# Kernel optimization log

Hardware: AMD Instinct MI355X
Metric: run time of the kernel (lower is better)

The kernel has to match this reference:

```python
import jax, jax.numpy as jnp
import numpy as np

N_NODES = 20000
N_EDGES = 320000
T = 8
C_IN = 32
C_OUT = 32
C_EDGE = 16


def setup_inputs() -> dict:
    key = jax.random.key(0)
    ks = jax.random.split(key, 10)

    def xavier(k, shape):
        fan_in, fan_out = shape[0], shape[1]
        limit = float(np.sqrt(6.0 / (fan_in + fan_out)))
        return jax.random.uniform(k, shape, jnp.float32, -limit, limit)

    X = jax.random.normal(ks[0], (N_NODES, T, C_IN), jnp.float32)
    edge_index = jax.random.randint(ks[1], (2, N_EDGES), 0, N_NODES, jnp.int32)
    edge_attr = jax.random.normal(ks[2], (N_EDGES, C_EDGE), jnp.float32)
    Wn1 = xavier(ks[3], (C_IN, C_OUT))
    We1 = xavier(ks[4], (C_EDGE, C_OUT))
    u1 = xavier(ks[5], (C_OUT, C_OUT))
    Wn2 = xavier(ks[6], (C_OUT, C_OUT))
    We2 = xavier(ks[7], (C_EDGE, C_OUT))
    u2 = xavier(ks[8], (C_OUT, C_OUT))
    return {"X": X, "edge_index": edge_index, "edge_attr": edge_attr,
            "Wn1": Wn1, "We1": We1, "u1": u1,
            "Wn2": Wn2, "We2": We2, "u2": u2}


def _gat_conv(x, edge_index, edge_attr, Wn, We, u):
    # x: [N, T, C_in] -> h: [N, T, C_out]
    h = jnp.matmul(x, Wn)
    _ea = jnp.matmul(edge_attr, We)  # computed in original forward, unused in message (dead code)
    # per-edge matmul with u == node-level matmul then gather (same math, cheaper)
    hu = jnp.matmul(h, u)  # [N, T, C]
    src, tgt = edge_index[0], edge_index[1]
    x_j = hu[src]  # [E, T, C]
    x_i = hu[tgt]  # [E, T, C]
    gate = jax.nn.sigmoid(jnp.sum(x_i * x_j, axis=-1, keepdims=True))  # [E, T, 1]
    msg = x_j * gate  # [E, T, C]
    agg = jax.ops.segment_max(msg, tgt, num_segments=N_NODES)  # max-aggregate into targets
    agg = jnp.where(jnp.isfinite(agg), agg, jnp.zeros((), agg.dtype))  # empty segments -> 0 (PyG fill)
    return h + agg  # residual update


def reference(X, edge_index, edge_attr, Wn1, We1, u1, Wn2, We2, u2):
    c1 = jax.nn.leaky_relu(_gat_conv(X, edge_index, edge_attr, Wn1, We1, u1), 0.01)
    c2 = jax.nn.leaky_relu(_gat_conv(c1, edge_index, edge_attr, Wn2, We2, u2), 0.01)
    return c2
```

## Files before the change

kernel.cpp:

```cpp
#include <hip/hip_runtime.h>
#include <hip/hip_fp16.h>
#include <cstdint>
#include <cstddef>
#include <math.h>

#define NNODES 20000
#define NEDGES 320000
#define TDIM   8
#define CDIM   32
#define RROWS  (NNODES * TDIM)
#define NELEM  (RROWS * CDIM)
#define ROWBLK (TDIM * CDIM)

static __device__ __forceinline__ float4 fmax4(float4 a, float4 b) {
    return make_float4(fmaxf(a.x, b.x), fmaxf(a.y, b.y),
                       fmaxf(a.z, b.z), fmaxf(a.w, b.w));
}

static __device__ __forceinline__ unsigned pk2(float a, float b) {
    __half2 h = __floats2half2_rn(a, b);
    return *reinterpret_cast<unsigned*>(&h);
}

static __device__ __forceinline__ float4 ld4h(const char* p) {
    uint2 v = *(const uint2*)p;
    __half2 h0 = *reinterpret_cast<__half2*>(&v.x);
    __half2 h1 = *reinterpret_cast<__half2*>(&v.y);
    float2 f0 = __half22float2(h0);
    float2 f1 = __half22float2(h1);
    return make_float4(f0.x, f0.y, f1.x, f1.y);
}

__global__ __launch_bounds__(1024) void wu_kernel(
    const float* __restrict__ W1, const float* __restrict__ U1, float* __restrict__ WU1,
    const float* __restrict__ W2, const float* __restrict__ U2, float* __restrict__ WU2)
{
    const float* W  = blockIdx.x ? W2  : W1;
    const float* U  = blockIdx.x ? U2  : U1;
    float*       WU = blockIdx.x ? WU2 : WU1;
    int t = threadIdx.x;
    int k = t >> 5, c = t & 31;
    float acc = 0.f;
#pragma unroll
    for (int j = 0; j < CDIM; ++j) acc = fmaf(W[k * CDIM + j], U[j * CDIM + c], acc);
    WU[k * CDIM + c] = acc;
}

__global__ __launch_bounds__(256) void linear2_kernel(
    const float* __restrict__ in,
    const float* __restrict__ W,
    const float* __restrict__ WU,
    float* __restrict__ h,
    __half* __restrict__ hu16)
{
    __shared__ float sx[64][33];
    int tid = threadIdx.x;
    int rowBase = blockIdx.x * 64;

    const float4* in4 = (const float4*)(in + (size_t)rowBase * CDIM);
#pragma unroll
    for (int i = 0; i < 2; ++i) {
        int idx = tid + i * 256;
        float4 v = in4[idx];
        int r = idx >> 3, q = idx & 7;
        sx[r][4 * q + 0] = v.x; sx[r][4 * q + 1] = v.y;
        sx[r][4 * q + 2] = v.z; sx[r][4 * q + 3] = v.w;
    }
    __syncthreads();

    int lane  = tid & 63;
    int chunk = __builtin_amdgcn_readfirstlane(tid >> 6);
    int row = rowBase + lane;

    float hr[8], acc[8];
#pragma unroll
    for (int j = 0; j < 8; ++j) { hr[j] = 0.f; acc[j] = 0.f; }

    const float* Wc  = W  + chunk * 8;
    const float* WUc = WU + chunk * 8;
#pragma unroll 4
    for (int k = 0; k < CDIM; ++k) {
        float xk = sx[lane][k];
#pragma unroll
        for (int j = 0; j < 8; ++j) {
            hr[j]  = fmaf(xk, Wc[k * CDIM + j],  hr[j]);
            acc[j] = fmaf(xk, WUc[k * CDIM + j], acc[j]);
        }
    }

    float* hp = h + (size_t)row * CDIM + chunk * 8;
    ((float4*)hp)[0] = make_float4(hr[0], hr[1], hr[2], hr[3]);
    ((float4*)hp)[1] = make_float4(hr[4], hr[5], hr[6], hr[7]);

    uint4* up = (uint4*)((char*)hu16 + (size_t)row * 64 + chunk * 16);
    *up = make_uint4(pk2(acc[0], acc[1]), pk2(acc[2], acc[3]),
                     pk2(acc[4], acc[5]), pk2(acc[6], acc[7]));
}

__global__ __launch_bounds__(256) void zero_counts_kernel(int* __restrict__ counts)
{
    int i = blockIdx.x * 256 + threadIdx.x;
    if (i < NNODES) counts[i] = 0;
}

__global__ __launch_bounds__(256) void hist_kernel(
    const int* __restrict__ ei, int* __restrict__ counts)
{
    int e = blockIdx.x * 256 + threadIdx.x;
    if (e < NEDGES) atomicAdd(&counts[ei[NEDGES + e]], 1);
}

__global__ __launch_bounds__(256) void blocksum_kernel(
    const int* __restrict__ counts, int* __restrict__ bsum)
{
    __shared__ int sd[256];
    int tid = threadIdx.x;
    int i = blockIdx.x * 256 + tid;
    sd[tid] = (i < NNODES) ? counts[i] : 0;
    __syncthreads();
#pragma unroll
    for (int off = 128; off > 0; off >>= 1) {
        if (tid < off) sd[tid] += sd[tid + off];
        __syncthreads();
    }
    if (tid == 0) bsum[blockIdx.x] = sd[0];
}

__global__ __launch_bounds__(128) void bscan_kernel(
    const int* __restrict__ bsum, int* __restrict__ bbase, int nblocks)
{
    __shared__ int sd[128];
    int tid = threadIdx.x;
    int v = (tid < nblocks) ? bsum[tid] : 0;
    sd[tid] = v;
    __syncthreads();
#pragma unroll
    for (int off = 1; off < 128; off <<= 1) {
        int t = (tid >= off) ? sd[tid - off] : 0;
        __syncthreads();
        sd[tid] += t;
        __syncthreads();
    }
    if (tid < nblocks) bbase[tid] = sd[tid] - v;
}

__global__ __launch_bounds__(256) void localscan_kernel(
    const int* __restrict__ counts, const int* __restrict__ bbase,
    int* __restrict__ offsets, int* __restrict__ cursor)
{
    __shared__ int sd[256];
    int tid = threadIdx.x;
    int i = blockIdx.x * 256 + tid;
    int v = (i < NNODES) ? counts[i] : 0;
    sd[tid] = v;
    __syncthreads();
#pragma unroll
    for (int off = 1; off < 256; off <<= 1) {
        int t = (tid >= off) ? sd[tid - off] : 0;
        __syncthreads();
        sd[tid] += t;
        __syncthreads();
    }
    int excl = bbase[blockIdx.x] + sd[tid] - v;
    if (i < NNODES) { offsets[i] = excl; cursor[i] = excl; }
    if (i == NNODES - 1) offsets[NNODES] = NEDGES;
}

__global__ __launch_bounds__(256) void scatter_kernel(
    const int* __restrict__ ei,
    int* __restrict__ cursor,
    int* __restrict__ csr_src)
{
    int e = blockIdx.x * 256 + threadIdx.x;
    if (e < NEDGES) {
        int t = ei[NEDGES + e];
        int pos = atomicAdd(&cursor[t], 1);
        csr_src[pos] = ei[e];
    }
}

__global__ __launch_bounds__(256) void agg_kernel(
    const int* __restrict__ offsets,
    const int* __restrict__ csr_src,
    const __half* __restrict__ hu16,
    const float* h,
    float* out)
{
    int tid = threadIdx.x;
    int n = blockIdx.x * 4 + (tid >> 6);
    int l64 = tid & 63;
    uint32_t rowOff = (uint32_t)l64 * 8u;
    const char* hub = (const char*)hu16;

    float4 bv = ld4h(hub + ((uint32_t)n << 9) + rowOff);

    int k0 = offsets[n];
    int k1 = offsets[n + 1];

    float4 m = make_float4(-INFINITY, -INFINITY, -INFINITY, -INFINITY);

    int k = k0;
    int kend4 = k0 + ((k1 - k0) & ~3);
    int s0, s1, s2, s3;
    if (k < kend4) {
        s0 = csr_src[k + 0]; s1 = csr_src[k + 1];
        s2 = csr_src[k + 2]; s3 = csr_src[k + 3];
    }
    while (k < kend4) {
        const char* p0 = hub + (((uint32_t)s0 << 9) + rowOff);
        const char* p1 = hub + (((uint32_t)s1 << 9) + rowOff);
        const char* p2 = hub + (((uint32_t)s2 << 9) + rowOff);
        const char* p3 = hub + (((uint32_t)s3 << 9) + rowOff);
        uint2 r0 = *(const uint2*)p0;
        uint2 r1 = *(const uint2*)p1;
        uint2 r2 = *(const uint2*)p2;
        uint2 r3 = *(const uint2*)p3;
        k += 4;
        if (k < kend4) {
            s0 = csr_src[k + 0]; s1 = csr_src[k + 1];
            s2 = csr_src[k + 2]; s3 = csr_src[k + 3];
        }
        float4 a0 = ld4h((const char*)&r0);
        float4 a1 = ld4h((const char*)&r1);
        float4 a2 = ld4h((const char*)&r2);
        float4 a3 = ld4h((const char*)&r3);
        float q0 = a0.x * bv.x + a0.y * bv.y + a0.z * bv.z + a0.w * bv.w;
        float q1 = a1.x * bv.x + a1.y * bv.y + a1.z * bv.z + a1.w * bv.w;
        float q2 = a2.x * bv.x + a2.y * bv.y + a2.z * bv.z + a2.w * bv.w;
        float q3 = a3.x * bv.x + a3.y * bv.y + a3.z * bv.z + a3.w * bv.w;
        q0 += __shfl_xor(q0, 1); q1 += __shfl_xor(q1, 1);
        q2 += __shfl_xor(q2, 1); q3 += __shfl_xor(q3, 1);
        q0 += __shfl_xor(q0, 2); q1 += __shfl_xor(q1, 2);
        q2 += __shfl_xor(q2, 2); q3 += __shfl_xor(q3, 2);
        q0 += __shfl_xor(q0, 4); q1 += __shfl_xor(q1, 4);
        q2 += __shfl_xor(q2, 4); q3 += __shfl_xor(q3, 4);
        float g0 = 1.f / (1.f + __expf(-q0));
        float g1 = 1.f / (1.f + __expf(-q1));
        float g2 = 1.f / (1.f + __expf(-q2));
        float g3 = 1.f / (1.f + __expf(-q3));
        m = fmax4(m, make_float4(a0.x * g0, a0.y * g0, a0.z * g0, a0.w * g0));
        m = fmax4(m, make_float4(a1.x * g1, a1.y * g1, a1.z * g1, a1.w * g1));
        m = fmax4(m, make_float4(a2.x * g2, a2.y * g2, a2.z * g2, a2.w * g2));
        m = fmax4(m, make_float4(a3.x * g3, a3.y * g3, a3.z * g3, a3.w * g3));
    }
    for (; k < k1; ++k) {
        int s = csr_src[k];
        float4 a0 = ld4h(hub + (((uint32_t)s << 9) + rowOff));
        float q0 = a0.x * bv.x + a0.y * bv.y + a0.z * bv.z + a0.w * bv.w;
        q0 += __shfl_xor(q0, 1);
        q0 += __shfl_xor(q0, 2);
        q0 += __shfl_xor(q0, 4);
        float g0 = 1.f / (1.f + __expf(-q0));
        m = fmax4(m, make_float4(a0.x * g0, a0.y * g0, a0.z * g0, a0.w * g0));
    }

    bool has = (k1 > k0);
    uint32_t nodeOff = (uint32_t)n * 1024u + (uint32_t)l64 * 16u;
    float4 hv = *(const float4*)((const char*)h + nodeOff);
    float ax = has ? m.x : 0.f;
    float ay = has ? m.y : 0.f;
    float az = has ? m.z : 0.f;
    float aw = has ? m.w : 0.f;
    float vx = hv.x + ax, vy = hv.y + ay, vz = hv.z + az, vw = hv.w + aw;
    float4 o;
    o.x = (vx >= 0.f) ? vx : 0.01f * vx;
    o.y = (vy >= 0.f) ? vy : 0.01f * vy;
    o.z = (vz >= 0.f) ? vz : 0.01f * vz;
    o.w = (vw >= 0.f) ? vw : 0.01f * vw;
    *(float4*)((char*)out + nodeOff) = o;
}

extern "C" void kernel_launch(void* const* d_in, const int* in_sizes, int n_in,
                              void* d_out, int out_size, void* d_ws, size_t ws_size,
                              hipStream_t stream)
{
    const float* X   = (const float*)d_in[0];
    const int*   ei  = (const int*)  d_in[1];
    const float* Wn1 = (const float*)d_in[3];
    const float* u1  = (const float*)d_in[5];
    const float* Wn2 = (const float*)d_in[6];
    const float* u2  = (const float*)d_in[8];

    float* out = (float*)d_out;

    int* counts  = (int*)d_ws;
    int* offsets = counts + NNODES;
    int* cursor  = offsets + NNODES + 1;
    int* bsum    = cursor + NNODES;
    int* bbase   = bsum + 128;
    float* WU1   = (float*)(bbase + 128);
    float* WU2   = WU1 + 1024;
    int* csr     = (int*)(WU2 + 1024);
    float*  A   = (float*)(((uintptr_t)(csr + NEDGES) + 255) & ~(uintptr_t)255);
    __half* H16 = (__half*)(A + NELEM);

    const int linBlocks  = RROWS / 64;
    const int edgeBlocks = (NEDGES + 255) / 256;
    const int nodeBlocks = (NNODES + 255) / 256;
    const int aggBlocks  = NNODES / 4;

    wu_kernel<<<2, 1024, 0, stream>>>(Wn1, u1, WU1, Wn2, u2, WU2);
    zero_counts_kernel<<<nodeBlocks, 256, 0, stream>>>(counts);
    hist_kernel<<<edgeBlocks, 256, 0, stream>>>(ei, counts);
    blocksum_kernel<<<nodeBlocks, 256, 0, stream>>>(counts, bsum);
    bscan_kernel<<<1, 128, 0, stream>>>(bsum, bbase, nodeBlocks);
    localscan_kernel<<<nodeBlocks, 256, 0, stream>>>(counts, bbase, offsets, cursor);
    scatter_kernel<<<edgeBlocks, 256, 0, stream>>>(ei, cursor, csr);

    linear2_kernel<<<linBlocks, 256, 0, stream>>>(X, Wn1, WU1, A, H16);
    agg_kernel<<<aggBlocks, 256, 0, stream>>>(offsets, csr, H16, A, A);

    linear2_kernel<<<linBlocks, 256, 0, stream>>>(A, Wn2, WU2, out, H16);
    agg_kernel<<<aggBlocks, 256, 0, stream>>>(offsets, csr, H16, out, out);
}
```

Measured before the change: 148.6 us.

## Fuse CSR build into cooperative kernel and widen agg loads to 16 bytes

Seven small launches (WU matmul, zero counts, histogram, block sums, block scan, local scan, scatter) are merged into one cooperative kernel that uses grid-wide syncs between phases. This removes per-launch gaps and the separate scan kernel. The aggregation kernel now has each lane load 16 bytes (8 halves), with the two wave halves handling alternate edges and combining their maxima through a cross-half shuffle. This halves the shuffle reduction depth per edge, at the cost of grid.sync overhead and idle half-waves in the epilogue.

```diff
diff --git a/kernel.cpp b/kernel.cpp
--- a/kernel.cpp
+++ b/kernel.cpp
@@ -1,8 +1,11 @@
 #include <hip/hip_runtime.h>
 #include <hip/hip_fp16.h>
+#include <hip/hip_cooperative_groups.h>
 #include <cstdint>
 #include <cstddef>
 #include <math.h>
+
+namespace cg = cooperative_groups;
 
 #define NNODES 20000
 #define NEDGES 320000
@@ -10,40 +13,97 @@
 #define CDIM   32
 #define RROWS  (NNODES * TDIM)
 #define NELEM  (RROWS * CDIM)
-#define ROWBLK (TDIM * CDIM)
-
-static __device__ __forceinline__ float4 fmax4(float4 a, float4 b) {
-    return make_float4(fmaxf(a.x, b.x), fmaxf(a.y, b.y),
-                       fmaxf(a.z, b.z), fmaxf(a.w, b.w));
-}
+
+#define CSR_GRID 256
+#define CSR_GT   (CSR_GRID * 256)
 
 static __device__ __forceinline__ unsigned pk2(float a, float b) {
     __half2 h = __floats2half2_rn(a, b);
     return *reinterpret_cast<unsigned*>(&h);
 }
 
-static __device__ __forceinline__ float4 ld4h(const char* p) {
-    uint2 v = *(const uint2*)p;
-    __half2 h0 = *reinterpret_cast<__half2*>(&v.x);
-    __half2 h1 = *reinterpret_cast<__half2*>(&v.y);
-    float2 f0 = __half22float2(h0);
-    float2 f1 = __half22float2(h1);
-    return make_float4(f0.x, f0.y, f1.x, f1.y);
-}
-
-__global__ __launch_bounds__(1024) void wu_kernel(
-    const float* __restrict__ W1, const float* __restrict__ U1, float* __restrict__ WU1,
-    const float* __restrict__ W2, const float* __restrict__ U2, float* __restrict__ WU2)
-{
-    const float* W  = blockIdx.x ? W2  : W1;
-    const float* U  = blockIdx.x ? U2  : U1;
-    float*       WU = blockIdx.x ? WU2 : WU1;
-    int t = threadIdx.x;
-    int k = t >> 5, c = t & 31;
-    float acc = 0.f;
-#pragma unroll
-    for (int j = 0; j < CDIM; ++j) acc = fmaf(W[k * CDIM + j], U[j * CDIM + c], acc);
-    WU[k * CDIM + c] = acc;
+static __device__ __forceinline__ void cvt8(uint4 r, float* a) {
+    float2 f;
+    f = __half22float2(*reinterpret_cast<__half2*>(&r.x)); a[0] = f.x; a[1] = f.y;
+    f = __half22float2(*reinterpret_cast<__half2*>(&r.y)); a[2] = f.x; a[3] = f.y;
+    f = __half22float2(*reinterpret_cast<__half2*>(&r.z)); a[4] = f.x; a[5] = f.y;
+    f = __half22float2(*reinterpret_cast<__half2*>(&r.w)); a[6] = f.x; a[7] = f.y;
+}
+
+__global__ __launch_bounds__(256) void csrwu_kernel(
+    const int* __restrict__ ei,
+    const float* __restrict__ Wn1, const float* __restrict__ u1, float* __restrict__ WU1,
+    const float* __restrict__ Wn2, const float* __restrict__ u2, float* __restrict__ WU2,
+    int* __restrict__ counts, int* __restrict__ offsets, int* __restrict__ cursor,
+    int* __restrict__ bsum, int* __restrict__ csr)
+{
+    cg::grid_group grid = cg::this_grid();
+    int blk = blockIdx.x, tid = threadIdx.x;
+    int gtid = blk * 256 + tid;
+    __shared__ int sd[256];
+
+    if (gtid < NNODES) counts[gtid] = 0;
+    if (blk < 8) {
+        const float* W  = (blk < 4) ? Wn1 : Wn2;
+        const float* U  = (blk < 4) ? u1  : u2;
+        float*       WU = (blk < 4) ? WU1 : WU2;
+        int idx = (blk & 3) * 256 + tid;
+        int k = idx >> 5, c = idx & 31;
+        float acc = 0.f;
+#pragma unroll
+        for (int j = 0; j < CDIM; ++j) acc = fmaf(W[k * CDIM + j], U[j * CDIM + c], acc);
+        WU[idx] = acc;
+    }
+    grid.sync();
+
+    for (int e = gtid; e < NEDGES; e += CSR_GT)
+        atomicAdd(&counts[ei[NEDGES + e]], 1);
+    grid.sync();
+
+    int v = 0;
+    if (blk < 79) {
+        v = (gtid < NNODES) ? counts[gtid] : 0;
+        sd[tid] = v;
+        __syncthreads();
+#pragma unroll
+        for (int off = 128; off > 0; off >>= 1) {
+            if (tid < off) sd[tid] += sd[tid + off];
+            __syncthreads();
+        }
+        if (tid == 0) bsum[blk] = sd[0];
+    }
+    grid.sync();
+
+    if (blk < 79) {
+        sd[tid] = (tid < blk) ? bsum[tid] : 0;
+        __syncthreads();
+#pragma unroll
+        for (int off = 128; off > 0; off >>= 1) {
+            if (tid < off) sd[tid] += sd[tid + off];
+            __syncthreads();
+        }
+        int base = sd[0];
+        __syncthreads();
+        sd[tid] = v;
+        __syncthreads();
+#pragma unroll
+        for (int off = 1; off < 256; off <<= 1) {
+            int t = (tid >= off) ? sd[tid - off] : 0;
+            __syncthreads();
+            sd[tid] += t;
+            __syncthreads();
+        }
+        int excl = base + sd[tid] - v;
+        if (gtid < NNODES) { offsets[gtid] = excl; cursor[gtid] = excl; }
+        if (gtid == NNODES - 1) offsets[NNODES] = NEDGES;
+    }
+    grid.sync();
+
+    for (int e = gtid; e < NEDGES; e += CSR_GT) {
+        int t = ei[NEDGES + e];
+        int pos = atomicAdd(&cursor[t], 1);
+        csr[pos] = ei[e];
+    }
 }
 
 __global__ __launch_bounds__(256) void linear2_kernel(
@@ -97,88 +157,6 @@
                      pk2(acc[4], acc[5]), pk2(acc[6], acc[7]));
 }
 
-__global__ __launch_bounds__(256) void zero_counts_kernel(int* __restrict__ counts)
-{
-    int i = blockIdx.x * 256 + threadIdx.x;
-    if (i < NNODES) counts[i] = 0;
-}
-
-__global__ __launch_bounds__(256) void hist_kernel(
-    const int* __restrict__ ei, int* __restrict__ counts)
-{
-    int e = blockIdx.x * 256 + threadIdx.x;
-    if (e < NEDGES) atomicAdd(&counts[ei[NEDGES + e]], 1);
-}
-
-__global__ __launch_bounds__(256) void blocksum_kernel(
-    const int* __restrict__ counts, int* __restrict__ bsum)
-{
-    __shared__ int sd[256];
-    int tid = threadIdx.x;
-    int i = blockIdx.x * 256 + tid;
-    sd[tid] = (i < NNODES) ? counts[i] : 0;
-    __syncthreads();
-#pragma unroll
-    for (int off = 128; off > 0; off >>= 1) {
-        if (tid < off) sd[tid] += sd[tid + off];
-        __syncthreads();
-    }
-    if (tid == 0) bsum[blockIdx.x] = sd[0];
-}
-
-__global__ __launch_bounds__(128) void bscan_kernel(
-    const int* __restrict__ bsum, int* __restrict__ bbase, int nblocks)
-{
-    __shared__ int sd[128];
-    int tid = threadIdx.x;
-    int v = (tid < nblocks) ? bsum[tid] : 0;
-    sd[tid] = v;
-    __syncthreads();
-#pragma unroll
-    for (int off = 1; off < 128; off <<= 1) {
-        int t = (tid >= off) ? sd[tid - off] : 0;
-        __syncthreads();
-        sd[tid] += t;
-        __syncthreads();
-    }
-    if (tid < nblocks) bbase[tid] = sd[tid] - v;
-}
-
-__global__ __launch_bounds__(256) void localscan_kernel(
-    const int* __restrict__ counts, const int* __restrict__ bbase,
-    int* __restrict__ offsets, int* __restrict__ cursor)
-{
-    __shared__ int sd[256];
-    int tid = threadIdx.x;
-    int i = blockIdx.x * 256 + tid;
-    int v = (i < NNODES) ? counts[i] : 0;
-    sd[tid] = v;
-    __syncthreads();
-#pragma unroll
-    for (int off = 1; off < 256; off <<= 1) {
-        int t = (tid >= off) ? sd[tid - off] : 0;
-        __syncthreads();
-        sd[tid] += t;
-        __syncthreads();
-    }
-    int excl = bbase[blockIdx.x] + sd[tid] - v;
-    if (i < NNODES) { offsets[i] = excl; cursor[i] = excl; }
-    if (i == NNODES - 1) offsets[NNODES] = NEDGES;
-}
-
-__global__ __launch_bounds__(256) void scatter_kernel(
-    const int* __restrict__ ei,
-    int* __restrict__ cursor,
-    int* __restrict__ csr_src)
-{
-    int e = blockIdx.x * 256 + threadIdx.x;
-    if (e < NEDGES) {
-        int t = ei[NEDGES + e];
-        int pos = atomicAdd(&cursor[t], 1);
-        csr_src[pos] = ei[e];
-    }
-}
-
 __global__ __launch_bounds__(256) void agg_kernel(
     const int* __restrict__ offsets,
     const int* __restrict__ csr_src,
@@ -189,93 +167,93 @@
     int tid = threadIdx.x;
     int n = blockIdx.x * 4 + (tid >> 6);
     int l64 = tid & 63;
-    uint32_t rowOff = (uint32_t)l64 * 8u;
+    int half = l64 >> 5;
+    int l32 = l64 & 31;
+    uint32_t rowOff = (uint32_t)l32 * 16u;
     const char* hub = (const char*)hu16;
 
-    float4 bv = ld4h(hub + ((uint32_t)n << 9) + rowOff);
+    float b[8];
+    cvt8(*(const uint4*)(hub + ((uint32_t)n << 9) + rowOff), b);
 
     int k0 = offsets[n];
     int k1 = offsets[n + 1];
 
-    float4 m = make_float4(-INFINITY, -INFINITY, -INFINITY, -INFINITY);
+    float m[8];
+#pragma unroll
+    for (int j = 0; j < 8; ++j) m[j] = -INFINITY;
 
     int k = k0;
-    int kend4 = k0 + ((k1 - k0) & ~3);
-    int s0, s1, s2, s3;
-    if (k < kend4) {
-        s0 = csr_src[k + 0]; s1 = csr_src[k + 1];
-        s2 = csr_src[k + 2]; s3 = csr_src[k + 3];
-    }
-    while (k < kend4) {
-        const char* p0 = hub + (((uint32_t)s0 << 9) + rowOff);
-        const char* p1 = hub + (((uint32_t)s1 << 9) + rowOff);
-        const char* p2 = hub + (((uint32_t)s2 << 9) + rowOff);
-        const char* p3 = hub + (((uint32_t)s3 << 9) + rowOff);
-        uint2 r0 = *(const uint2*)p0;
-        uint2 r1 = *(const uint2*)p1;
-        uint2 r2 = *(const uint2*)p2;
-        uint2 r3 = *(const uint2*)p3;
+    int e0 = 0, e1 = 0;
+    if (k + 4 <= k1) {
+        e0 = csr_src[k + half];
+        e1 = csr_src[k + 2 + half];
+    }
+    while (k + 4 <= k1) {
+        uint4 r0 = *(const uint4*)(hub + (((uint32_t)e0 << 9) + rowOff));
+        uint4 r1 = *(const uint4*)(hub + (((uint32_t)e1 << 9) + rowOff));
         k += 4;
-        if (k < kend4) {
-            s0 = csr_src[k + 0]; s1 = csr_src[k + 1];
-            s2 = csr_src[k + 2]; s3 = csr_src[k + 3];
-        }
-        float4 a0 = ld4h((const char*)&r0);
-        float4 a1 = ld4h((const char*)&r1);
-        float4 a2 = ld4h((const char*)&r2);
-        float4 a3 = ld4h((const char*)&r3);
-        float q0 = a0.x * bv.x + a0.y * bv.y + a0.z * bv.z + a0.w * bv.w;
-        float q1 = a1.x * bv.x + a1.y * bv.y + a1.z * bv.z + a1.w * bv.w;
-        float q2 = a2.x * bv.x + a2.y * bv.y + a2.z * bv.z + a2.w * bv.w;
-        float q3 = a3.x * bv.x + a3.y * bv.y + a3.z * bv.z + a3.w * bv.w;
+        if (k + 4 <= k1) {
+            e0 = csr_src[k + half];
+            e1 = csr_src[k + 2 + half];
+        }
+        float a0[8], a1[8];
+        cvt8(r0, a0); cvt8(r1, a1);
+        float q0 = 0.f, q1 = 0.f;
+#pragma unroll
+        for (int j = 0; j < 8; ++j) { q0 = fmaf(a0[j], b[j], q0); q1 = fmaf(a1[j], b[j], q1); }
         q0 += __shfl_xor(q0, 1); q1 += __shfl_xor(q1, 1);
-        q2 += __shfl_xor(q2, 1); q3 += __shfl_xor(q3, 1);
         q0 += __shfl_xor(q0, 2); q1 += __shfl_xor(q1, 2);
-        q2 += __shfl_xor(q2, 2); q3 += __shfl_xor(q3, 2);
-        q0 += __shfl_xor(q0, 4); q1 += __shfl_xor(q1, 4);
-        q2 += __shfl_xor(q2, 4); q3 += __shfl_xor(q3, 4);
         float g0 = 1.f / (1.f + __expf(-q0));
         float g1 = 1.f / (1.f + __expf(-q1));
-        float g2 = 1.f / (1.f + __expf(-q2));
-        float g3 = 1.f / (1.f + __expf(-q3));
-        m = fmax4(m, make_float4(a0.x * g0, a0.y * g0, a0.z * g0, a0.w * g0));
-        m = fmax4(m, make_float4(a1.x * g1, a1.y * g1, a1.z * g1, a1.w * g1));
-        m = fmax4(m, make_float4(a2.x * g2, a2.y * g2, a2.z * g2, a2.w * g2));
-        m = fmax4(m, make_float4(a3.x * g3, a3.y * g3, a3.z * g3, a3.w * g3));
+#pragma unroll
+        for (int j = 0; j < 8; ++j) {
+            m[j] = fmaxf(m[j], a0[j] * g0);
+            m[j] = fmaxf(m[j], a1[j] * g1);
+        }
     }
     for (; k < k1; ++k) {
         int s = csr_src[k];
-        float4 a0 = ld4h(hub + (((uint32_t)s << 9) + rowOff));
-        float q0 = a0.x * bv.x + a0.y * bv.y + a0.z * bv.z + a0.w * bv.w;
+        float a0[8];
+        cvt8(*(const uint4*)(hub + (((uint32_t)s << 9) + rowOff)), a0);
+        float q0 = 0.f;
+#pragma unroll
+        for (int j = 0; j < 8; ++j) q0 = fmaf(a0[j], b[j], q0);
         q0 += __shfl_xor(q0, 1);
         q0 += __shfl_xor(q0, 2);
-        q0 += __shfl_xor(q0, 4);
         float g0 = 1.f / (1.f + __expf(-q0));
-        m = fmax4(m, make_float4(a0.x * g0, a0.y * g0, a0.z * g0, a0.w * g0));
-    }
-
-    bool has = (k1 > k0);
-    uint32_t nodeOff = (uint32_t)n * 1024u + (uint32_t)l64 * 16u;
-    float4 hv = *(const float4*)((const char*)h + nodeOff);
-    float ax = has ? m.x : 0.f;
-    float ay = has ? m.y : 0.f;
-    float az = has ? m.z : 0.f;
-    float aw = has ? m.w : 0.f;
-    float vx = hv.x + ax, vy = hv.y + ay, vz = hv.z + az, vw = hv.w + aw;
-    float4 o;
-    o.x = (vx >= 0.f) ? vx : 0.01f * vx;
-    o.y = (vy >= 0.f) ? vy : 0.01f * vy;
-    o.z = (vz >= 0.f) ? vz : 0.01f * vz;
-    o.w = (vw >= 0.f) ? vw : 0.01f * vw;
-    *(float4*)((char*)out + nodeOff) = o;
+#pragma unroll
+        for (int j = 0; j < 8; ++j) m[j] = fmaxf(m[j], a0[j] * g0);
+    }
+
+#pragma unroll
+    for (int j = 0; j < 8; ++j) m[j] = fmaxf(m[j], __shfl_xor(m[j], 32));
+
+    if (half == 0) {
+        bool has = (k1 > k0);
+        uint32_t nodeOff = (uint32_t)n * 1024u + (uint32_t)l32 * 32u;
+        const char* hb = (const char*)h;
+        float4 hv0 = *(const float4*)(hb + nodeOff);
+        float4 hv1 = *(const float4*)(hb + nodeOff + 16);
+        float o[8];
+        float hvv[8] = {hv0.x, hv0.y, hv0.z, hv0.w, hv1.x, hv1.y, hv1.z, hv1.w};
+#pragma unroll
+        for (int j = 0; j < 8; ++j) {
+            float a = has ? m[j] : 0.f;
+            float vv = hvv[j] + a;
+            o[j] = (vv >= 0.f) ? vv : 0.01f * vv;
+        }
+        char* ob = (char*)out;
+        *(float4*)(ob + nodeOff)      = make_float4(o[0], o[1], o[2], o[3]);
+        *(float4*)(ob + nodeOff + 16) = make_float4(o[4], o[5], o[6], o[7]);
+    }
 }
 
 extern "C" void kernel_launch(void* const* d_in, const int* in_sizes, int n_in,
                               void* d_out, int out_size, void* d_ws, size_t ws_size,
                               hipStream_t stream)
 {
+    const int*   ei  = (const int*)  d_in[1];
     const float* X   = (const float*)d_in[0];
-    const int*   ei  = (const int*)  d_in[1];
     const float* Wn1 = (const float*)d_in[3];
     const float* u1  = (const float*)d_in[5];
     const float* Wn2 = (const float*)d_in[6];
@@ -287,25 +265,24 @@
     int* offsets = counts + NNODES;
     int* cursor  = offsets + NNODES + 1;
     int* bsum    = cursor + NNODES;
-    int* bbase   = bsum + 128;
-    float* WU1   = (float*)(bbase + 128);
+    float* WU1   = (float*)(bsum + 128);
     float* WU2   = WU1 + 1024;
     int* csr     = (int*)(WU2 + 1024);
     float*  A   = (float*)(((uintptr_t)(csr + NEDGES) + 255) & ~(uintptr_t)255);
     __half* H16 = (__half*)(A + NELEM);
 
-    const int linBlocks  = RROWS / 64;
-    const int edgeBlocks = (NEDGES + 255) / 256;
-    const int nodeBlocks = (NNODES + 255) / 256;
-    const int aggBlocks  = NNODES / 4;
-
-    wu_kernel<<<2, 1024, 0, stream>>>(Wn1, u1, WU1, Wn2, u2, WU2);
-    zero_counts_kernel<<<nodeBlocks, 256, 0, stream>>>(counts);
-    hist_kernel<<<edgeBlocks, 256, 0, stream>>>(ei, counts);
-    blocksum_kernel<<<nodeBlocks, 256, 0, stream>>>(counts, bsum);
-    bscan_kernel<<<1, 128, 0, stream>>>(bsum, bbase, nodeBlocks);
-    localscan_kernel<<<nodeBlocks, 256, 0, stream>>>(counts, bbase, offsets, cursor);
-    scatter_kernel<<<edgeBlocks, 256, 0, stream>>>(ei, cursor, csr);
+    const int linBlocks = RROWS / 64;
+    const int aggBlocks = NNODES / 4;
+
+    void* args[] = {
+        (void*)&ei,
+        (void*)&Wn1, (void*)&u1, (void*)&WU1,
+        (void*)&Wn2, (void*)&u2, (void*)&WU2,
+        (void*)&counts, (void*)&offsets, (void*)&cursor,
+        (void*)&bsum, (void*)&csr
+    };
+    hipLaunchCooperativeKernel((const void*)csrwu_kernel,
+                               dim3(CSR_GRID), dim3(256), args, 0, stream);
 
     linear2_kernel<<<linBlocks, 256, 0, stream>>>(X, Wn1, WU1, A, H16);
     agg_kernel<<<aggBlocks, 256, 0, stream>>>(offsets, csr, H16, A, A);
```

Result: slower. 248.8 us (+67.4%).
